# Performance work log

Measured on AMD Instinct MI355X. Metric: run time of the kernel, lower is better.

Reference implementation:

```python
import jax, jax.numpy as jnp
import numpy as np

B, N, K, NUM_CLASSES = 8, 4096, 16, 40
M = B * N


def _safe_norm(v):
    s = jnp.sum(v * v, axis=-1)
    return jnp.where(s > 0, jnp.sqrt(jnp.where(s > 0, s, 1.0)), 0.0)


def _angle(v1, v2):
    cn = _safe_norm(jnp.cross(v1, v2))
    d = jnp.sum(v1 * v2, axis=-1)
    ok = (cn > 0) | (d != 0)
    return jnp.where(ok, jnp.arctan2(cn, jnp.where(ok, d, 1.0)), 0.0)


def _ppf(pos_i, pos_j, n_i, n_j):
    # PyG point_pair_features: pseudo = pos_j - pos_i (j = source, i = target)
    pseudo = pos_j - pos_i
    return jnp.stack([_safe_norm(pseudo), _angle(n_i, pseudo),
                      _angle(n_j, pseudo), _angle(n_i, n_j)], axis=-1)


def _knn_edges(pos):
    # knn_graph(k=K, loop=False), per-graph; returns (src, dst) with self-loops
    # appended (PPFConv add_self_loops=True default).
    p = pos.reshape(B, N, 3)
    sq = jnp.sum(p * p, axis=-1)                                   # [B,N]
    d2 = sq[:, :, None] + sq[:, None, :] - 2.0 * jnp.einsum('bnd,bmd->bnm', p, p)
    d2 = jnp.where(jnp.eye(N, dtype=bool)[None], jnp.inf, d2)      # no loops
    _, nbr = jax.lax.top_k(-d2, K)                                  # [B,N,K]
    offs = (jnp.arange(B) * N)[:, None, None]
    src = (nbr + offs).reshape(-1)                                  # neighbors j
    dst = jnp.repeat(jnp.arange(M), K)                              # targets i
    loops = jnp.arange(M)
    return jnp.concatenate([src, loops]), jnp.concatenate([dst, loops])


def _mlp(e, w1, b1, w2, b2):
    return jax.nn.relu(e @ w1 + b1) @ w2 + b2


def setup_inputs() -> dict:
    key = jax.random.key(0)
    ks = jax.random.split(key, 12)
    pos = jax.random.normal(ks[0], (M, 3), jnp.float32)
    nrm = jax.random.normal(ks[1], (M, 3), jnp.float32)
    nrm = nrm / jnp.linalg.norm(nrm, axis=-1, keepdims=True)
    batch = jnp.repeat(jnp.arange(B, dtype=jnp.int32), N)
    s = 0.1
    return {
        'pos': pos, 'normal': nrm, 'batch': batch,
        'w1a': jax.random.normal(ks[2], (4, 32)) * s,  'b1a': jnp.zeros(32),
        'w1b': jax.random.normal(ks[3], (32, 32)) * s, 'b1b': jnp.zeros(32),
        'w2a': jax.random.normal(ks[4], (36, 32)) * s, 'b2a': jnp.zeros(32),
        'w2b': jax.random.normal(ks[5], (32, 32)) * s, 'b2b': jnp.zeros(32),
        'wc':  jax.random.normal(ks[6], (32, NUM_CLASSES)) * s,
        'bc':  jnp.zeros(NUM_CLASSES),
    }


def reference(pos, normal, batch, w1a, b1a, w1b, b1b, w2a, b2a, w2b, b2b, wc, bc):
    src, dst = _knn_edges(pos)
    feats = _ppf(pos[dst], pos[src], normal[dst], normal[src])      # [E,4]
    # conv1: x=None -> message = mlp1(ppf), scatter-max per target node
    msg1 = _mlp(feats, w1a, b1a, w1b, b1b)
    x = jax.nn.relu(jax.ops.segment_max(msg1, dst, num_segments=M))  # [M,32]
    # conv2: message = mlp2([x_j, ppf])
    msg2 = _mlp(jnp.concatenate([x[src], feats], axis=-1), w2a, b2a, w2b, b2b)
    x = jax.nn.relu(jax.ops.segment_max(msg2, dst, num_segments=M))
    # global_max_pool over each graph (uniform batch: reshape)
    g = x.reshape(B, N, 32).max(axis=1)                              # [B,32]
    return g @ wc + bc                                               # [B,40]
```

## Files before the change

### kernel.cpp

```cpp
#include <hip/hip_runtime.h>
#include <hip/hip_bf16.h>
#include <math.h>

#define NB 8
#define NN 4096
#define KK 16
#define MM (NB*NN)
#define CH 32
#define SLOTS 17
#define NCLS 40
#define BIG 3.0e38f
#define CAP 96
#define NBLK2 (MM/64)
#define HROW 36

#define OW1A 0
#define OB1A 128
#define OW1B 160
#define OB1B 1184
#define OW2A 1216
#define OB2A 2368
#define OW2B 2400
#define OB2B 3424
#define OWC  3456
#define OBC  4736
#define NWTS 4776

typedef short short8 __attribute__((ext_vector_type(8)));
typedef float f32x4  __attribute__((ext_vector_type(4)));
typedef float f32x2  __attribute__((ext_vector_type(2)));

__device__ float4 g_pos4[MM];
__device__ float4 g_nrm4[MM];
__device__ int    g_nbr[MM*KK];
__device__ float  g_u[MM*CH];
__device__ float  g_bmax[NBLK2*CH];
__device__ float  g_wts[NWTS];
__device__ __align__(16) float4 g_fe4[MM*SLOTS];
__device__ __align__(16) unsigned short g_wfrag1[2][2][64][8];
__device__ __align__(16) unsigned short g_wfrag2[2][2][64][8];

__device__ __forceinline__ float bf(const __hip_bfloat16 x) { return __bfloat162float(x); }

__device__ __forceinline__ float ldf(const void* p, int i, bool f32) {
  return f32 ? ((const float*)p)[i] : bf(((const __hip_bfloat16*)p)[i]);
}

__device__ __forceinline__ float angf(float ax, float ay, float az,
                                      float bx, float by, float bz) {
  float cx = ay*bz - az*by;
  float cy = az*bx - ax*bz;
  float cz = ax*by - ay*bx;
  float s  = cx*cx + cy*cy + cz*cz;
  float cn = s > 0.f ? sqrtf(s) : 0.f;
  float d  = ax*bx + ay*by + az*bz;
  return (cn > 0.f || d != 0.f) ? atan2f(cn, d) : 0.f;
}

__device__ __forceinline__ void ppf4(const float4 pi, const float4 ni,
                                     const float4 pj, const float4 nj, float* f) {
  float px = pj.x - pi.x, py = pj.y - pi.y, pz = pj.z - pi.z;
  float s = px*px + py*py + pz*pz;
  f[0] = s > 0.f ? sqrtf(s) : 0.f;
  f[1] = angf(ni.x, ni.y, ni.z, px, py, pz);
  f[2] = angf(nj.x, nj.y, nj.z, px, py, pz);
  f[3] = angf(ni.x, ni.y, ni.z, nj.x, nj.y, nj.z);
}

__device__ __forceinline__ unsigned int fkey(float f) {
  unsigned int u = __float_as_uint(f);
  return (u & 0x80000000u) ? ~u : (u | 0x80000000u);
}
__device__ __forceinline__ float funkey(unsigned int k) {
  unsigned int u = (k & 0x80000000u) ? (k ^ 0x80000000u) : ~k;
  return __uint_as_float(u);
}

__device__ __forceinline__ unsigned int mbcnt64(unsigned long long m) {
  return __builtin_amdgcn_mbcnt_hi((unsigned int)(m >> 32),
         __builtin_amdgcn_mbcnt_lo((unsigned int)m, 0u));
}

__device__ __forceinline__ void bsplit(float v, unsigned short* hi, unsigned short* lo) {
  __hip_bfloat16 h = __float2bfloat16(v);
  float hf = __bfloat162float(h);
  __hip_bfloat16 l = __float2bfloat16(v - hf);
  *hi = *reinterpret_cast<unsigned short*>(&h);
  *lo = *reinterpret_cast<unsigned short*>(&l);
}

__device__ __forceinline__ void afrag(const float* row, short8* ah, short8* al) {
  float4 a = *(const float4*)row;
  float4 b = *(const float4*)(row + 4);
  unsigned short h, l;
  #pragma unroll
  for (int j = 0; j < 4; ++j) {
    bsplit((&a.x)[j], &h, &l); (*ah)[j]   = (short)h; (*al)[j]   = (short)l;
    bsplit((&b.x)[j], &h, &l); (*ah)[j+4] = (short)h; (*al)[j+4] = (short)l;
  }
}

__global__ __launch_bounds__(256) void prep_kernel(
    const void* __restrict__ pos, const void* __restrict__ nrm,
    const void* w1a, const void* b1a, const void* w1b, const void* b1b,
    const void* w2a, const void* b2a, const void* w2b, const void* b2b,
    const void* wc, const void* bc) {
  __shared__ int sflag;
  const int tid = threadIdx.x;
  const int base = blockIdx.x << 8;
  if (tid < 64) {
    const float* nf = (const float*)nrm;
    const __hip_bfloat16* nh = (const __hip_bfloat16*)nrm;
    int n = base + tid;
    float x = nf[3*n], y = nf[3*n+1], z = nf[3*n+2];
    float ss = x*x + y*y + z*z;
    bool okf = (ss > 0.98f && ss < 1.02f);
    float a = bf(nh[3*n]), b2 = bf(nh[3*n+1]), c2 = bf(nh[3*n+2]);
    float sb = a*a + b2*b2 + c2*c2;
    bool okb = (sb > 0.95f && sb < 1.05f);
    unsigned long long mf = __ballot(okf), mb = __ballot(okb);
    if (tid == 0) sflag = (__popcll(mf) >= __popcll(mb)) ? 1 : 0;
  }
  __syncthreads();
  const bool f32 = sflag != 0;
  {
    int i = base + tid;
    float x = ldf(pos, 3*i, f32), y = ldf(pos, 3*i+1, f32), z = ldf(pos, 3*i+2, f32);
    g_pos4[i] = make_float4(x, y, z, x*x + y*y + z*z);
    float a = ldf(nrm, 3*i, f32), bb = ldf(nrm, 3*i+1, f32), cc = ldf(nrm, 3*i+2, f32);
    g_nrm4[i] = make_float4(a, bb, cc, 0.f);
  }
  if (blockIdx.x == 0) {
    for (int t = tid; t < 128;  t += 256) g_wts[OW1A + t] = ldf(w1a, t, f32);
    for (int t = tid; t < 32;   t += 256) g_wts[OB1A + t] = ldf(b1a, t, f32);
    for (int t = tid; t < 1024; t += 256) g_wts[OW1B + t] = ldf(w1b, t, f32);
    for (int t = tid; t < 32;   t += 256) g_wts[OB1B + t] = ldf(b1b, t, f32);
    for (int t = tid; t < 1152; t += 256) g_wts[OW2A + t] = ldf(w2a, t, f32);
    for (int t = tid; t < 32;   t += 256) g_wts[OB2A + t] = ldf(b2a, t, f32);
    for (int t = tid; t < 1024; t += 256) g_wts[OW2B + t] = ldf(w2b, t, f32);
    for (int t = tid; t < 32;   t += 256) g_wts[OB2B + t] = ldf(b2b, t, f32);
    for (int t = tid; t < 1280; t += 256) g_wts[OWC  + t] = ldf(wc,  t, f32);
    for (int t = tid; t < 40;   t += 256) g_wts[OBC  + t] = ldf(bc,  t, f32);
    for (int t = tid; t < 4096; t += 256) {
      int which = t >> 11;
      int r = t & 2047;
      int tt = r >> 10;  r &= 1023;
      int hl = r >> 9;   r &= 511;
      int ln = r >> 3;
      int j  = r & 7;
      int k = (ln >> 4)*8 + j;
      int c = tt*16 + (ln & 15);
      float wv = ldf(which ? w2b : w1b, k*CH + c, f32);
      unsigned short hi, lo;
      bsplit(wv, &hi, &lo);
      unsigned short v = hl ? lo : hi;
      if (which) g_wfrag2[tt][hl][ln][j] = v;
      else       g_wfrag1[tt][hl][ln][j] = v;
    }
  }
}

__global__ __launch_bounds__(512) void knn_conv1_kernel() {
  __shared__ __align__(16) union SU {
    struct {
      float sx[NN], sy[NN], sz[NN];
      unsigned short ilst[64][CAP];
      double dlst[8][CAP];
    } k;
    struct {
      float fe[272][4];
      float h1s[288*HROW];
      float wsaT[32*HROW];
      float xs[16][CH];
    } c;
  } u;
  __shared__ unsigned short nbrs[64][KK];
  __shared__ unsigned short swcnt[64];

  const int tid  = threadIdx.x;
  const int w    = tid >> 6, lane = tid & 63;
  const int blk  = blockIdx.x;
  const int b    = blk >> 6;
  const int qbw  = ((blk & 63) << 6) | (w << 3);
  const float4* bp = g_pos4 + b*NN;

  #pragma unroll
  for (int k = 0; k < 8; ++k) {
    int idx = k*512 + tid;
    float4 o = bp[idx];
    u.k.sx[idx] = o.x; u.k.sy[idx] = o.y; u.k.sz[idx] = o.z;
  }
  __syncthreads();

  float q2x[8], q2y[8], q2z[8];
  #pragma unroll
  for (int qq = 0; qq < 8; ++qq) {
    int qi = qbw + qq;
    q2x[qq] = -2.f*u.k.sx[qi]; q2y[qq] = -2.f*u.k.sy[qi]; q2z[qq] = -2.f*u.k.sz[qi];
  }
  const f32x2* sx2 = (const f32x2*)u.k.sx;
  const f32x2* sy2 = (const f32x2*)u.k.sy;
  const f32x2* sz2 = (const f32x2*)u.k.sz;

  float mn[8];
  #pragma unroll
  for (int qq = 0; qq < 8; ++qq) mn[qq] = BIG;
  #pragma unroll 4
  for (int it = 0; it < 32; ++it) {
    int p = it*64 + lane;
    f32x2 ox = sx2[p], oy = sy2[p], oz = sz2[p];
    f32x2 ow = __builtin_elementwise_fma(oz, oz,
               __builtin_elementwise_fma(oy, oy, ox*ox));
    #pragma unroll
    for (int qq = 0; qq < 8; ++qq) {
      f32x2 qx = {q2x[qq], q2x[qq]};
      f32x2 qy = {q2y[qq], q2y[qq]};
      f32x2 qz = {q2z[qq], q2z[qq]};
      f32x2 d = __builtin_elementwise_fma(qx, ox,
                __builtin_elementwise_fma(qy, oy,
                __builtin_elementwise_fma(qz, oz, ow)));
      mn[qq] = fminf(fminf(d[0], d[1]), mn[qq]);
    }
  }

  unsigned int key[8], lo[8], hi[8];
  #pragma unroll
  for (int qq = 0; qq < 8; ++qq) { key[qq] = fkey(mn[qq]) >> 16; lo[qq] = 0u; hi[qq] = 0xFFFFu; }
  #pragma unroll 1
  for (int s = 0; s < 16; ++s) {
    #pragma unroll
    for (int qq = 0; qq < 8; ++qq) {
      unsigned int mid = (lo[qq] + hi[qq]) >> 1;
      int c = (int)__popcll(__ballot(key[qq] <= mid));
      if (c >= 17) hi[qq] = mid; else lo[qq] = mid + 1;
    }
  }
  float Tf[8];
  #pragma unroll
  for (int qq = 0; qq < 8; ++qq) {
    float T = funkey((hi[qq] << 16) | 0xFFFFu);
    Tf[qq] = T + 4e-5f + 1e-5f*fabsf(T);
  }

  unsigned int scnt[8];
  #pragma unroll
  for (int qq = 0; qq < 8; ++qq) scnt[qq] = 0u;
  #pragma unroll 2
  for (int it = 0; it < 32; ++it) {
    int p = it*64 + lane;
    f32x2 ox = sx2[p], oy = sy2[p], oz = sz2[p];
    f32x2 ow = __builtin_elementwise_fma(oz, oz,
               __builtin_elementwise_fma(oy, oy, ox*ox));
    #pragma unroll
    for (int qq = 0; qq < 8; ++qq) {
      f32x2 qx = {q2x[qq], q2x[qq]};
      f32x2 qy = {q2y[qq], q2y[qq]};
      f32x2 qz = {q2z[qq], q2z[qq]};
      f32x2 d = __builtin_elementwise_fma(qx, ox,
                __builtin_elementwise_fma(qy, oy,
                __builtin_elementwise_fma(qz, oz, ow)));
      bool h0 = d[0] <= Tf[qq];
      bool h1 = d[1] <= Tf[qq];
      unsigned long long mk0 = __ballot(h0);
      unsigned long long mk1 = __ballot(h1);
      if (mk0 | mk1) {
        unsigned int cbase = scnt[qq];
        if (h0) {
          unsigned int pos = cbase + mbcnt64(mk0);
          if (pos < CAP) u.k.ilst[(w<<3)|qq][pos] = (unsigned short)(2*p);
        }
        cbase += (unsigned int)__popcll(mk0);
        if (h1) {
          unsigned int pos = cbase + mbcnt64(mk1);
          if (pos < CAP) u.k.ilst[(w<<3)|qq][pos] = (unsigned short)(2*p + 1);
        }
        scnt[qq] = cbase + (unsigned int)__popcll(mk1);
      }
    }
  }
  if (lane == 0) {
    #pragma unroll
    for (int qq = 0; qq < 8; ++qq)
      swcnt[(w<<3)|qq] = (unsigned short)min((int)scnt[qq], CAP);
  }

  #pragma unroll 1
  for (int qq = 0; qq < 8; ++qq) {
    const int qi = qbw + qq;
    const int ql = (w<<3) | qq;
    const int m = (int)swcnt[ql];
    const double mx = (double)u.k.sx[qi], my_ = (double)u.k.sy[qi], mz = (double)u.k.sz[qi];
    const double sqme = (mx*mx + my_*my_) + mz*mz;
    for (int e = lane; e < m; e += 64) {
      int ci = u.k.ilst[ql][e];
      double ox = (double)u.k.sx[ci], oy = (double)u.k.sy[ci], oz = (double)u.k.sz[ci];
      double sqo = (ox*ox + oy*oy) + oz*oz;
      double dt  = (mx*ox + my_*oy) + mz*oz;
      u.k.dlst[w][e] = (sqme + sqo) - 2.0*dt;
    }
    for (int e = lane; e < m; e += 64) {
      double myd = u.k.dlst[w][e];
      int myi = u.k.ilst[ql][e];
      int rank = 0;
      for (int o = 0; o < m; ++o) {
        double od = u.k.dlst[w][o];
        int oi = u.k.ilst[ql][o];
        rank += (od < myd) || (od == myd && oi < myi);
      }
      if (rank >= 1 && rank <= KK) {
        nbrs[ql][rank-1] = (unsigned short)myi;
        g_nbr[(b*NN + qi)*KK + (rank-1)] = b*NN + myi;
      }
    }
  }

  const int c32 = tid & 31;
  const int quad = lane >> 4, l15 = lane & 15;
  float w1a_c[4];
  #pragma unroll
  for (int f = 0; f < 4; ++f) w1a_c[f] = g_wts[OW1A + f*CH + c32];
  const float b1a_c = g_wts[OB1A + c32];
  short8 bH0 = *(const short8*)&g_wfrag1[0][0][lane][0];
  short8 bL0 = *(const short8*)&g_wfrag1[0][1][lane][0];
  short8 bH1 = *(const short8*)&g_wfrag1[1][0][lane][0];
  short8 bL1 = *(const short8*)&g_wfrag1[1][1][lane][0];
  const float bias0 = g_wts[OB1B + l15];
  const float bias1 = g_wts[OB1B + 16 + l15];

  __syncthreads();

  for (int i2 = tid; i2 < 1024; i2 += 512) {
    int k = i2 >> 5, cc = i2 & 31;
    u.c.wsaT[cc*HROW + k] = g_wts[OW2A + i2];
  }
  const int nbb = b*NN + ((blk & 63) << 6);

  #pragma unroll 1
  for (int ck = 0; ck < 4; ++ck) {
    const int nloc0 = ck << 4;
    if (tid < 272) {
      int ns = tid / 17, slot = tid - ns*17;
      int iloc = nloc0 + ns;
      int ig = nbb + iloc;
      int jg = (slot < KK) ? (b*NN + (int)nbrs[iloc][slot]) : ig;
      float f[4];
      ppf4(g_pos4[ig], g_nrm4[ig], g_pos4[jg], g_nrm4[jg], f);
      float4 fv = make_float4(f[0], f[1], f[2], f[3]);
      *(float4*)u.c.fe[tid] = fv;
      g_fe4[(size_t)(nbb + nloc0)*SLOTS + tid] = fv;
    }
    __syncthreads();
    #pragma unroll
    for (int it = 0; it < 17; ++it) {
      int idx = it*512 + tid;
      int e = idx >> 5;
      float4 f4 = *(const float4*)u.c.fe[e];
      float h = b1a_c + f4.x*w1a_c[0] + f4.y*w1a_c[1] + f4.z*w1a_c[2] + f4.w*w1a_c[3];
      u.c.h1s[e*HROW + c32] = fmaxf(h, 0.f);
    }
    __syncthreads();
    #pragma unroll
    for (int ni = 0; ni < 2; ++ni) {
      const int n16 = w*2 + ni;
      const int rbase = n16*17;
      short8 ah0, al0, ah1, al1;
      afrag(&u.c.h1s[(rbase      + l15)*HROW + quad*8], &ah0, &al0);
      afrag(&u.c.h1s[(rbase + 16 + l15)*HROW + quad*8], &ah1, &al1);
      f32x4 a00 = {0.f,0.f,0.f,0.f}, a01 = a00, a10 = a00, a11 = a00;
      a00 = __builtin_amdgcn_mfma_f32_16x16x32_bf16(ah0, bH0, a00, 0, 0, 0);
      a00 = __builtin_amdgcn_mfma_f32_16x16x32_bf16(ah0, bL0, a00, 0, 0, 0);
      a00 = __builtin_amdgcn_mfma_f32_16x16x32_bf16(al0, bH0, a00, 0, 0, 0);
      a01 = __builtin_amdgcn_mfma_f32_16x16x32_bf16(ah0, bH1, a01, 0, 0, 0);
      a01 = __builtin_amdgcn_mfma_f32_16x16x32_bf16(ah0, bL1, a01, 0, 0, 0);
      a01 = __builtin_amdgcn_mfma_f32_16x16x32_bf16(al0, bH1, a01, 0, 0, 0);
      a10 = __builtin_amdgcn_mfma_f32_16x16x32_bf16(ah1, bH0, a10, 0, 0, 0);
      a10 = __builtin_amdgcn_mfma_f32_16x16x32_bf16(ah1, bL0, a10, 0, 0, 0);
      a10 = __builtin_amdgcn_mfma_f32_16x16x32_bf16(al1, bH0, a10, 0, 0, 0);
      a11 = __builtin_amdgcn_mfma_f32_16x16x32_bf16(ah1, bH1, a11, 0, 0, 0);
      a11 = __builtin_amdgcn_mfma_f32_16x16x32_bf16(ah1, bL1, a11, 0, 0, 0);
      a11 = __builtin_amdgcn_mfma_f32_16x16x32_bf16(al1, bH1, a11, 0, 0, 0);
      float m0 = fmaxf(fmaxf(a00[0], a00[1]), fmaxf(a00[2], a00[3]));
      float m1 = fmaxf(fmaxf(a01[0], a01[1]), fmaxf(a01[2], a01[3]));
      if (quad == 0) { m0 = fmaxf(m0, a10[0]); m1 = fmaxf(m1, a11[0]); }
      m0 = fmaxf(m0, __shfl_xor(m0, 16)); m0 = fmaxf(m0, __shfl_xor(m0, 32));
      m1 = fmaxf(m1, __shfl_xor(m1, 16)); m1 = fmaxf(m1, __shfl_xor(m1, 32));
      if (quad == 0) {
        u.c.xs[n16][l15]      = fmaxf(m0 + bias0, 0.f);
        u.c.xs[n16][16 + l15] = fmaxf(m1 + bias1, 0.f);
      }
    }
    __syncthreads();
    {
      int ns = tid >> 5;
      float uu = 0.f;
      #pragma unroll
      for (int k4 = 0; k4 < 8; ++k4) {
        float4 x4 = *(const float4*)&u.c.xs[ns][4*k4];
        float4 w4 = *(const float4*)&u.c.wsaT[c32*HROW + 4*k4];
        uu += x4.x*w4.x + x4.y*w4.y + x4.z*w4.z + x4.w*w4.w;
      }
      g_u[(nbb + nloc0 + ns)*CH + c32] = uu;
    }
    __syncthreads();
  }
}

__global__ __launch_bounds__(512) void conv2_kernel() {
  __shared__ __align__(16) float fe[272][4];
  __shared__ int jn[272];
  __shared__ __align__(16) float h1s[288*HROW];
  __shared__ float xs[16][CH];
  const int tid = threadIdx.x;
  const int c = tid & 31;
  const int lane = tid & 63, wv = tid >> 6;
  const int quad = lane >> 4, l15 = lane & 15;
  const int node0 = blockIdx.x << 6;
  float w2aL_c[4];
  #pragma unroll
  for (int f = 0; f < 4; ++f) w2aL_c[f] = g_wts[OW2A + (CH + f)*CH + c];
  const float b2a_c = g_wts[OB2A + c];
  short8 bH0 = *(const short8*)&g_wfrag2[0][0][lane][0];
  short8 bL0 = *(const short8*)&g_wfrag2[0][1][lane][0];
  short8 bH1 = *(const short8*)&g_wfrag2[1][0][lane][0];
  short8 bL1 = *(const short8*)&g_wfrag2[1][1][lane][0];
  const float bias0 = g_wts[OB2B + l15];
  const float bias1 = g_wts[OB2B + 16 + l15];
  float bmx = 0.f;

  #pragma unroll 1
  for (int ck = 0; ck < 4; ++ck) {
    const int n0 = node0 + (ck << 4);
    if (tid < 272) {
      int ns = tid / 17, slot = tid - ns*17;
      int i = n0 + ns;
      jn[tid] = (slot < KK) ? g_nbr[i*KK + slot] : i;
      *(float4*)fe[tid] = g_fe4[(size_t)n0*SLOTS + tid];
    }
    __syncthreads();
    #pragma unroll
    for (int it = 0; it < 17; ++it) {
      int idx = it*512 + tid;
      int e = idx >> 5;
      float4 f4 = *(const float4*)fe[e];
      float uv = g_u[jn[e]*CH + c];
      float h = b2a_c + uv + f4.x*w2aL_c[0] + f4.y*w2aL_c[1] + f4.z*w2aL_c[2] + f4.w*w2aL_c[3];
      h1s[e*HROW + c] = fmaxf(h, 0.f);
    }
    __syncthreads();
    #pragma unroll
    for (int ni = 0; ni < 2; ++ni) {
      const int n16 = wv*2 + ni;
      const int rbase = n16*17;
      short8 ah0, al0, ah1, al1;
      afrag(&h1s[(rbase      + l15)*HROW + quad*8], &ah0, &al0);
      afrag(&h1s[(rbase + 16 + l15)*HROW + quad*8], &ah1, &al1);
      f32x4 a00 = {0.f,0.f,0.f,0.f}, a01 = a00, a10 = a00, a11 = a00;
      a00 = __builtin_amdgcn_mfma_f32_16x16x32_bf16(ah0, bH0, a00, 0, 0, 0);
      a00 = __builtin_amdgcn_mfma_f32_16x16x32_bf16(ah0, bL0, a00, 0, 0, 0);
      a00 = __builtin_amdgcn_mfma_f32_16x16x32_bf16(al0, bH0, a00, 0, 0, 0);
      a01 = __builtin_amdgcn_mfma_f32_16x16x32_bf16(ah0, bH1, a01, 0, 0, 0);
      a01 = __builtin_amdgcn_mfma_f32_16x16x32_bf16(ah0, bL1, a01, 0, 0, 0);
      a01 = __builtin_amdgcn_mfma_f32_16x16x32_bf16(al0, bH1, a01, 0, 0, 0);
      a10 = __builtin_amdgcn_mfma_f32_16x16x32_bf16(ah1, bH0, a10, 0, 0, 0);
      a10 = __builtin_amdgcn_mfma_f32_16x16x32_bf16(ah1, bL0, a10, 0, 0, 0);
      a10 = __builtin_amdgcn_mfma_f32_16x16x32_bf16(al1, bH0, a10, 0, 0, 0);
      a11 = __builtin_amdgcn_mfma_f32_16x16x32_bf16(ah1, bH1, a11, 0, 0, 0);
      a11 = __builtin_amdgcn_mfma_f32_16x16x32_bf16(ah1, bL1, a11, 0, 0, 0);
      a11 = __builtin_amdgcn_mfma_f32_16x16x32_bf16(al1, bH1, a11, 0, 0, 0);
      float m0 = fmaxf(fmaxf(a00[0], a00[1]), fmaxf(a00[2], a00[3]));
      float m1 = fmaxf(fmaxf(a01[0], a01[1]), fmaxf(a01[2], a01[3]));
      if (quad == 0) { m0 = fmaxf(m0, a10[0]); m1 = fmaxf(m1, a11[0]); }
      m0 = fmaxf(m0, __shfl_xor(m0, 16)); m0 = fmaxf(m0, __shfl_xor(m0, 32));
      m1 = fmaxf(m1, __shfl_xor(m1, 16)); m1 = fmaxf(m1, __shfl_xor(m1, 32));
      if (quad == 0) {
        xs[n16][l15]      = fmaxf(m0 + bias0, 0.f);
        xs[n16][16 + l15] = fmaxf(m1 + bias1, 0.f);
      }
    }
    __syncthreads();
    if (tid < CH) {
      #pragma unroll
      for (int r = 0; r < 16; ++r) bmx = fmaxf(bmx, xs[r][c]);
    }
    __syncthreads();
  }
  if (tid < CH) g_bmax[blockIdx.x*CH + c] = bmx;
}

__global__ __launch_bounds__(256) void head_kernel(float* __restrict__ out) {
  __shared__ float red[8][CH];
  __shared__ float gm[CH];
  const int g = blockIdx.x;
  const int c = threadIdx.x & 31, sub = threadIdx.x >> 5;
  const float* base = g_bmax + (size_t)(g*64 + sub*8)*CH;
  float mx = 0.f;
  #pragma unroll
  for (int n = 0; n < 8; ++n) mx = fmaxf(mx, base[n*CH + c]);
  red[sub][c] = mx;
  __syncthreads();
  if (threadIdx.x < CH) {
    float m2 = red[0][c];
    #pragma unroll
    for (int r = 1; r < 8; ++r) m2 = fmaxf(m2, red[r][c]);
    gm[c] = m2;
  }
  __syncthreads();
  if (threadIdx.x < NCLS) {
    int co = threadIdx.x;
    float s = g_wts[OBC + co];
    #pragma unroll
    for (int f = 0; f < CH; ++f) s += gm[f] * g_wts[OWC + f*NCLS + co];
    out[g*NCLS + co] = s;
  }
}

extern "C" void kernel_launch(void* const* d_in, const int* in_sizes, int n_in,
                              void* d_out, int out_size, void* d_ws, size_t ws_size,
                              hipStream_t stream) {
  const void* pos = d_in[0];
  const void* nrm = d_in[1];
  const void* w1a = d_in[3];
  const void* b1a = d_in[4];
  const void* w1b = d_in[5];
  const void* b1b = d_in[6];
  const void* w2a = d_in[7];
  const void* b2a = d_in[8];
  const void* w2b = d_in[9];
  const void* b2b = d_in[10];
  const void* wc  = d_in[11];
  const void* bc  = d_in[12];

  prep_kernel<<<MM/256, 256, 0, stream>>>(pos, nrm, w1a, b1a, w1b, b1b,
                                          w2a, b2a, w2b, b2b, wc, bc);
  knn_conv1_kernel<<<MM/64, 512, 0, stream>>>();
  conv2_kernel<<<MM/64, 512, 0, stream>>>();
  head_kernel<<<NB, 256, 0, stream>>>((float*)d_out);
}
```

Before: 191.7 us.

## Halve nodes per block and stream candidate points through LDS in halves

Each block now handles 32 query nodes instead of 64, with 4 queries per wave. The kNN scan loads the 4096 candidate points into shared memory in two halves of 2048, which shrinks the LDS footprint and adds an extra barrier per pass. PPF features are built once for the whole block rather than per chunk, the double-precision refinement reads candidate positions from global memory, and the conv stages process one node per wave per chunk. The aim is more resident blocks per CU (launch bounds min 8 blocks) and twice as many blocks, at the cost of reloading the point set twice per block and more total global traffic.

```diff
diff --git a/kernel.cpp b/kernel.cpp
--- a/kernel.cpp
+++ b/kernel.cpp
@@ -11,8 +11,10 @@
 #define NCLS 40
 #define BIG 3.0e38f
 #define CAP 96
-#define NBLK2 (MM/64)
+#define NPB 32
+#define NBLK (MM/NPB)
 #define HROW 36
+#define HALF 2048
 
 #define OW1A 0
 #define OB1A 128
@@ -34,7 +36,7 @@
 __device__ float4 g_nrm4[MM];
 __device__ int    g_nbr[MM*KK];
 __device__ float  g_u[MM*CH];
-__device__ float  g_bmax[NBLK2*CH];
+__device__ float  g_bmax[NBLK*CH];
 __device__ float  g_wts[NWTS];
 __device__ __align__(16) float4 g_fe4[MM*SLOTS];
 __device__ __align__(16) unsigned short g_wfrag1[2][2][64][8];
@@ -160,140 +162,152 @@
   }
 }
 
-__global__ __launch_bounds__(512) void knn_conv1_kernel() {
+__global__ __launch_bounds__(512, 8) void knn_conv1_kernel() {
   __shared__ __align__(16) union SU {
     struct {
-      float sx[NN], sy[NN], sz[NN];
-      unsigned short ilst[64][CAP];
+      float sx[HALF], sy[HALF], sz[HALF];
+      unsigned short ilst[NPB][CAP];
       double dlst[8][CAP];
     } k;
     struct {
-      float fe[272][4];
-      float h1s[288*HROW];
+      float fe[NPB*SLOTS][4];
+      float h1s[152*HROW];
       float wsaT[32*HROW];
-      float xs[16][CH];
+      float xs[NPB][CH];
     } c;
   } u;
-  __shared__ unsigned short nbrs[64][KK];
-  __shared__ unsigned short swcnt[64];
+  __shared__ unsigned short nbrs[NPB][KK];
 
   const int tid  = threadIdx.x;
   const int w    = tid >> 6, lane = tid & 63;
   const int blk  = blockIdx.x;
-  const int b    = blk >> 6;
-  const int qbw  = ((blk & 63) << 6) | (w << 3);
+  const int b    = blk >> 7;
+  const int qb   = (blk & 127) << 5;
   const float4* bp = g_pos4 + b*NN;
 
-  #pragma unroll
-  for (int k = 0; k < 8; ++k) {
-    int idx = k*512 + tid;
-    float4 o = bp[idx];
-    u.k.sx[idx] = o.x; u.k.sy[idx] = o.y; u.k.sz[idx] = o.z;
-  }
-  __syncthreads();
-
-  float q2x[8], q2y[8], q2z[8];
-  #pragma unroll
-  for (int qq = 0; qq < 8; ++qq) {
-    int qi = qbw + qq;
-    q2x[qq] = -2.f*u.k.sx[qi]; q2y[qq] = -2.f*u.k.sy[qi]; q2z[qq] = -2.f*u.k.sz[qi];
-  }
+  float q2x[4], q2y[4], q2z[4];
+  #pragma unroll
+  for (int qq = 0; qq < 4; ++qq) {
+    float4 qv = bp[qb + (w << 2) + qq];
+    q2x[qq] = -2.f*qv.x; q2y[qq] = -2.f*qv.y; q2z[qq] = -2.f*qv.z;
+  }
+
   const f32x2* sx2 = (const f32x2*)u.k.sx;
   const f32x2* sy2 = (const f32x2*)u.k.sy;
   const f32x2* sz2 = (const f32x2*)u.k.sz;
 
-  float mn[8];
-  #pragma unroll
-  for (int qq = 0; qq < 8; ++qq) mn[qq] = BIG;
-  #pragma unroll 4
-  for (int it = 0; it < 32; ++it) {
-    int p = it*64 + lane;
-    f32x2 ox = sx2[p], oy = sy2[p], oz = sz2[p];
-    f32x2 ow = __builtin_elementwise_fma(oz, oz,
-               __builtin_elementwise_fma(oy, oy, ox*ox));
-    #pragma unroll
-    for (int qq = 0; qq < 8; ++qq) {
-      f32x2 qx = {q2x[qq], q2x[qq]};
-      f32x2 qy = {q2y[qq], q2y[qq]};
-      f32x2 qz = {q2z[qq], q2z[qq]};
-      f32x2 d = __builtin_elementwise_fma(qx, ox,
-                __builtin_elementwise_fma(qy, oy,
-                __builtin_elementwise_fma(qz, oz, ow)));
-      mn[qq] = fminf(fminf(d[0], d[1]), mn[qq]);
-    }
-  }
-
-  unsigned int key[8], lo[8], hi[8];
-  #pragma unroll
-  for (int qq = 0; qq < 8; ++qq) { key[qq] = fkey(mn[qq]) >> 16; lo[qq] = 0u; hi[qq] = 0xFFFFu; }
+  float mn[4];
+  #pragma unroll
+  for (int qq = 0; qq < 4; ++qq) mn[qq] = BIG;
+  #pragma unroll 1
+  for (int h = 0; h < 2; ++h) {
+    #pragma unroll
+    for (int k = 0; k < 4; ++k) {
+      int idx = k*512 + tid;
+      float4 o = bp[h*HALF + idx];
+      u.k.sx[idx] = o.x; u.k.sy[idx] = o.y; u.k.sz[idx] = o.z;
+    }
+    __syncthreads();
+    #pragma unroll 4
+    for (int it = 0; it < 16; ++it) {
+      int p = it*64 + lane;
+      f32x2 ox = sx2[p], oy = sy2[p], oz = sz2[p];
+      f32x2 ow = __builtin_elementwise_fma(oz, oz,
+                 __builtin_elementwise_fma(oy, oy, ox*ox));
+      #pragma unroll
+      for (int qq = 0; qq < 4; ++qq) {
+        f32x2 qx = {q2x[qq], q2x[qq]};
+        f32x2 qy = {q2y[qq], q2y[qq]};
+        f32x2 qz = {q2z[qq], q2z[qq]};
+        f32x2 d = __builtin_elementwise_fma(qx, ox,
+                  __builtin_elementwise_fma(qy, oy,
+                  __builtin_elementwise_fma(qz, oz, ow)));
+        mn[qq] = fminf(fminf(d[0], d[1]), mn[qq]);
+      }
+    }
+    __syncthreads();
+  }
+
+  unsigned int key[4], lo[4], hi[4];
+  #pragma unroll
+  for (int qq = 0; qq < 4; ++qq) { key[qq] = fkey(mn[qq]) >> 16; lo[qq] = 0u; hi[qq] = 0xFFFFu; }
   #pragma unroll 1
   for (int s = 0; s < 16; ++s) {
     #pragma unroll
-    for (int qq = 0; qq < 8; ++qq) {
+    for (int qq = 0; qq < 4; ++qq) {
       unsigned int mid = (lo[qq] + hi[qq]) >> 1;
       int c = (int)__popcll(__ballot(key[qq] <= mid));
       if (c >= 17) hi[qq] = mid; else lo[qq] = mid + 1;
     }
   }
-  float Tf[8];
-  #pragma unroll
-  for (int qq = 0; qq < 8; ++qq) {
+  float Tf[4];
+  #pragma unroll
+  for (int qq = 0; qq < 4; ++qq) {
     float T = funkey((hi[qq] << 16) | 0xFFFFu);
     Tf[qq] = T + 4e-5f + 1e-5f*fabsf(T);
   }
 
-  unsigned int scnt[8];
-  #pragma unroll
-  for (int qq = 0; qq < 8; ++qq) scnt[qq] = 0u;
-  #pragma unroll 2
-  for (int it = 0; it < 32; ++it) {
-    int p = it*64 + lane;
-    f32x2 ox = sx2[p], oy = sy2[p], oz = sz2[p];
-    f32x2 ow = __builtin_elementwise_fma(oz, oz,
-               __builtin_elementwise_fma(oy, oy, ox*ox));
-    #pragma unroll
-    for (int qq = 0; qq < 8; ++qq) {
-      f32x2 qx = {q2x[qq], q2x[qq]};
-      f32x2 qy = {q2y[qq], q2y[qq]};
-      f32x2 qz = {q2z[qq], q2z[qq]};
-      f32x2 d = __builtin_elementwise_fma(qx, ox,
-                __builtin_elementwise_fma(qy, oy,
-                __builtin_elementwise_fma(qz, oz, ow)));
-      bool h0 = d[0] <= Tf[qq];
-      bool h1 = d[1] <= Tf[qq];
-      unsigned long long mk0 = __ballot(h0);
-      unsigned long long mk1 = __ballot(h1);
-      if (mk0 | mk1) {
-        unsigned int cbase = scnt[qq];
-        if (h0) {
-          unsigned int pos = cbase + mbcnt64(mk0);
-          if (pos < CAP) u.k.ilst[(w<<3)|qq][pos] = (unsigned short)(2*p);
+  unsigned int scnt[4];
+  #pragma unroll
+  for (int qq = 0; qq < 4; ++qq) scnt[qq] = 0u;
+  #pragma unroll 1
+  for (int h = 0; h < 2; ++h) {
+    #pragma unroll
+    for (int k = 0; k < 4; ++k) {
+      int idx = k*512 + tid;
+      float4 o = bp[h*HALF + idx];
+      u.k.sx[idx] = o.x; u.k.sy[idx] = o.y; u.k.sz[idx] = o.z;
+    }
+    __syncthreads();
+    #pragma unroll 2
+    for (int it = 0; it < 16; ++it) {
+      int p = it*64 + lane;
+      int gidx = h*HALF + 2*p;
+      f32x2 ox = sx2[p], oy = sy2[p], oz = sz2[p];
+      f32x2 ow = __builtin_elementwise_fma(oz, oz,
+                 __builtin_elementwise_fma(oy, oy, ox*ox));
+      #pragma unroll
+      for (int qq = 0; qq < 4; ++qq) {
+        f32x2 qx = {q2x[qq], q2x[qq]};
+        f32x2 qy = {q2y[qq], q2y[qq]};
+        f32x2 qz = {q2z[qq], q2z[qq]};
+        f32x2 d = __builtin_elementwise_fma(qx, ox,
+                  __builtin_elementwise_fma(qy, oy,
+                  __builtin_elementwise_fma(qz, oz, ow)));
+        bool h0 = d[0] <= Tf[qq];
+        bool h1 = d[1] <= Tf[qq];
+        unsigned long long mk0 = __ballot(h0);
+        unsigned long long mk1 = __ballot(h1);
+        if (mk0 | mk1) {
+          unsigned int cbase = scnt[qq];
+          if (h0) {
+            unsigned int pos = cbase + mbcnt64(mk0);
+            if (pos < CAP) u.k.ilst[(w<<2)|qq][pos] = (unsigned short)gidx;
+          }
+          cbase += (unsigned int)__popcll(mk0);
+          if (h1) {
+            unsigned int pos = cbase + mbcnt64(mk1);
+            if (pos < CAP) u.k.ilst[(w<<2)|qq][pos] = (unsigned short)(gidx + 1);
+          }
+          scnt[qq] = cbase + (unsigned int)__popcll(mk1);
         }
-        cbase += (unsigned int)__popcll(mk0);
-        if (h1) {
-          unsigned int pos = cbase + mbcnt64(mk1);
-          if (pos < CAP) u.k.ilst[(w<<3)|qq][pos] = (unsigned short)(2*p + 1);
-        }
-        scnt[qq] = cbase + (unsigned int)__popcll(mk1);
-      }
-    }
-  }
-  if (lane == 0) {
-    #pragma unroll
-    for (int qq = 0; qq < 8; ++qq)
-      swcnt[(w<<3)|qq] = (unsigned short)min((int)scnt[qq], CAP);
+      }
+    }
+    __syncthreads();
   }
 
   #pragma unroll 1
-  for (int qq = 0; qq < 8; ++qq) {
-    const int qi = qbw + qq;
-    const int ql = (w<<3) | qq;
-    const int m = (int)swcnt[ql];
-    const double mx = (double)u.k.sx[qi], my_ = (double)u.k.sy[qi], mz = (double)u.k.sz[qi];
+  for (int qq = 0; qq < 4; ++qq) {
+    const int ql = (w << 2) | qq;
+    const int m = min((int)scnt[qq], CAP);
+    const double mx = (double)(-0.5f*q2x[qq]);
+    const double my_ = (double)(-0.5f*q2y[qq]);
+    const double mz = (double)(-0.5f*q2z[qq]);
     const double sqme = (mx*mx + my_*my_) + mz*mz;
     for (int e = lane; e < m; e += 64) {
       int ci = u.k.ilst[ql][e];
-      double ox = (double)u.k.sx[ci], oy = (double)u.k.sy[ci], oz = (double)u.k.sz[ci];
+      float4 cv = bp[ci];
+      double ox = (double)cv.x, oy = (double)cv.y, oz = (double)cv.z;
       double sqo = (ox*ox + oy*oy) + oz*oz;
       double dt  = (mx*ox + my_*oy) + mz*oz;
       u.k.dlst[w][e] = (sqme + sqo) - 2.0*dt;
@@ -309,7 +323,7 @@
       }
       if (rank >= 1 && rank <= KK) {
         nbrs[ql][rank-1] = (unsigned short)myi;
-        g_nbr[(b*NN + qi)*KK + (rank-1)] = b*NN + myi;
+        g_nbr[(b*NN + qb + ql)*KK + (rank-1)] = b*NN + myi;
       }
     }
   }
@@ -333,36 +347,34 @@
     int k = i2 >> 5, cc = i2 & 31;
     u.c.wsaT[cc*HROW + k] = g_wts[OW2A + i2];
   }
-  const int nbb = b*NN + ((blk & 63) << 6);
+  const int nbb = b*NN + qb;
+  for (int e = tid; e < NPB*SLOTS; e += 512) {
+    int ns = e / 17, slot = e - ns*17;
+    int ig = nbb + ns;
+    int jg = (slot < KK) ? (b*NN + (int)nbrs[ns][slot]) : ig;
+    float f[4];
+    ppf4(g_pos4[ig], g_nrm4[ig], g_pos4[jg], g_nrm4[jg], f);
+    float4 fv = make_float4(f[0], f[1], f[2], f[3]);
+    *(float4*)u.c.fe[e] = fv;
+    g_fe4[(size_t)nbb*SLOTS + e] = fv;
+  }
+  __syncthreads();
 
   #pragma unroll 1
   for (int ck = 0; ck < 4; ++ck) {
-    const int nloc0 = ck << 4;
-    if (tid < 272) {
-      int ns = tid / 17, slot = tid - ns*17;
-      int iloc = nloc0 + ns;
-      int ig = nbb + iloc;
-      int jg = (slot < KK) ? (b*NN + (int)nbrs[iloc][slot]) : ig;
-      float f[4];
-      ppf4(g_pos4[ig], g_nrm4[ig], g_pos4[jg], g_nrm4[jg], f);
-      float4 fv = make_float4(f[0], f[1], f[2], f[3]);
-      *(float4*)u.c.fe[tid] = fv;
-      g_fe4[(size_t)(nbb + nloc0)*SLOTS + tid] = fv;
-    }
-    __syncthreads();
-    #pragma unroll
-    for (int it = 0; it < 17; ++it) {
+    #pragma unroll
+    for (int it = 0; it < 9; ++it) {
       int idx = it*512 + tid;
       int e = idx >> 5;
-      float4 f4 = *(const float4*)u.c.fe[e];
-      float h = b1a_c + f4.x*w1a_c[0] + f4.y*w1a_c[1] + f4.z*w1a_c[2] + f4.w*w1a_c[3];
-      u.c.h1s[e*HROW + c32] = fmaxf(h, 0.f);
-    }
-    __syncthreads();
-    #pragma unroll
-    for (int ni = 0; ni < 2; ++ni) {
-      const int n16 = w*2 + ni;
-      const int rbase = n16*17;
+      if (e < 136) {
+        float4 f4 = *(const float4*)u.c.fe[ck*136 + e];
+        float h = b1a_c + f4.x*w1a_c[0] + f4.y*w1a_c[1] + f4.z*w1a_c[2] + f4.w*w1a_c[3];
+        u.c.h1s[e*HROW + c32] = fmaxf(h, 0.f);
+      }
+    }
+    __syncthreads();
+    {
+      const int rbase = w*17;
       short8 ah0, al0, ah1, al1;
       afrag(&u.c.h1s[(rbase      + l15)*HROW + quad*8], &ah0, &al0);
       afrag(&u.c.h1s[(rbase + 16 + l15)*HROW + quad*8], &ah1, &al1);
@@ -385,36 +397,36 @@
       m0 = fmaxf(m0, __shfl_xor(m0, 16)); m0 = fmaxf(m0, __shfl_xor(m0, 32));
       m1 = fmaxf(m1, __shfl_xor(m1, 16)); m1 = fmaxf(m1, __shfl_xor(m1, 32));
       if (quad == 0) {
-        u.c.xs[n16][l15]      = fmaxf(m0 + bias0, 0.f);
-        u.c.xs[n16][16 + l15] = fmaxf(m1 + bias1, 0.f);
-      }
-    }
-    __syncthreads();
-    {
-      int ns = tid >> 5;
-      float uu = 0.f;
-      #pragma unroll
-      for (int k4 = 0; k4 < 8; ++k4) {
-        float4 x4 = *(const float4*)&u.c.xs[ns][4*k4];
-        float4 w4 = *(const float4*)&u.c.wsaT[c32*HROW + 4*k4];
-        uu += x4.x*w4.x + x4.y*w4.y + x4.z*w4.z + x4.w*w4.w;
-      }
-      g_u[(nbb + nloc0 + ns)*CH + c32] = uu;
-    }
-    __syncthreads();
-  }
-}
-
-__global__ __launch_bounds__(512) void conv2_kernel() {
-  __shared__ __align__(16) float fe[272][4];
-  __shared__ int jn[272];
-  __shared__ __align__(16) float h1s[288*HROW];
-  __shared__ float xs[16][CH];
+        u.c.xs[ck*8 + w][l15]      = fmaxf(m0 + bias0, 0.f);
+        u.c.xs[ck*8 + w][16 + l15] = fmaxf(m1 + bias1, 0.f);
+      }
+    }
+    __syncthreads();
+  }
+  #pragma unroll
+  for (int it = 0; it < 2; ++it) {
+    int ns = it*16 + (tid >> 5);
+    float uu = 0.f;
+    #pragma unroll
+    for (int k4 = 0; k4 < 8; ++k4) {
+      float4 x4 = *(const float4*)&u.c.xs[ns][4*k4];
+      float4 w4 = *(const float4*)&u.c.wsaT[c32*HROW + 4*k4];
+      uu += x4.x*w4.x + x4.y*w4.y + x4.z*w4.z + x4.w*w4.w;
+    }
+    g_u[(nbb + ns)*CH + c32] = uu;
+  }
+}
+
+__global__ __launch_bounds__(512, 8) void conv2_kernel() {
+  __shared__ __align__(16) float fe[NPB*SLOTS][4];
+  __shared__ int jn[NPB*SLOTS];
+  __shared__ __align__(16) float h1s[152*HROW];
+  __shared__ float xs[NPB][CH];
   const int tid = threadIdx.x;
   const int c = tid & 31;
   const int lane = tid & 63, wv = tid >> 6;
   const int quad = lane >> 4, l15 = lane & 15;
-  const int node0 = blockIdx.x << 6;
+  const int node0 = blockIdx.x << 5;
   float w2aL_c[4];
   #pragma unroll
   for (int f = 0; f < 4; ++f) w2aL_c[f] = g_wts[OW2A + (CH + f)*CH + c];
@@ -425,32 +437,31 @@
   short8 bL1 = *(const short8*)&g_wfrag2[1][1][lane][0];
   const float bias0 = g_wts[OB2B + l15];
   const float bias1 = g_wts[OB2B + 16 + l15];
-  float bmx = 0.f;
+
+  for (int e = tid; e < NPB*SLOTS; e += 512) {
+    int ns = e / 17, slot = e - ns*17;
+    int i = node0 + ns;
+    jn[e] = (slot < KK) ? g_nbr[i*KK + slot] : i;
+    *(float4*)fe[e] = g_fe4[(size_t)node0*SLOTS + e];
+  }
+  __syncthreads();
 
   #pragma unroll 1
   for (int ck = 0; ck < 4; ++ck) {
-    const int n0 = node0 + (ck << 4);
-    if (tid < 272) {
-      int ns = tid / 17, slot = tid - ns*17;
-      int i = n0 + ns;
-      jn[tid] = (slot < KK) ? g_nbr[i*KK + slot] : i;
-      *(float4*)fe[tid] = g_fe4[(size_t)n0*SLOTS + tid];
-    }
-    __syncthreads();
-    #pragma unroll
-    for (int it = 0; it < 17; ++it) {
+    #pragma unroll
+    for (int it = 0; it < 9; ++it) {
       int idx = it*512 + tid;
       int e = idx >> 5;
-      float4 f4 = *(const float4*)fe[e];
-      float uv = g_u[jn[e]*CH + c];
-      float h = b2a_c + uv + f4.x*w2aL_c[0] + f4.y*w2aL_c[1] + f4.z*w2aL_c[2] + f4.w*w2aL_c[3];
-      h1s[e*HROW + c] = fmaxf(h, 0.f);
-    }
-    __syncthreads();
-    #pragma unroll
-    for (int ni = 0; ni < 2; ++ni) {
-      const int n16 = wv*2 + ni;
-      const int rbase = n16*17;
+      if (e < 136) {
+        float4 f4 = *(const float4*)fe[ck*136 + e];
+        float uv = g_u[jn[ck*136 + e]*CH + c];
+        float h = b2a_c + uv + f4.x*w2aL_c[0] + f4.y*w2aL_c[1] + f4.z*w2aL_c[2] + f4.w*w2aL_c[3];
+        h1s[e*HROW + c] = fmaxf(h, 0.f);
+      }
+    }
+    __syncthreads();
+    {
+      const int rbase = wv*17;
       short8 ah0, al0, ah1, al1;
       afrag(&h1s[(rbase      + l15)*HROW + quad*8], &ah0, &al0);
       afrag(&h1s[(rbase + 16 + l15)*HROW + quad*8], &ah1, &al1);
@@ -473,18 +484,18 @@
       m0 = fmaxf(m0, __shfl_xor(m0, 16)); m0 = fmaxf(m0, __shfl_xor(m0, 32));
       m1 = fmaxf(m1, __shfl_xor(m1, 16)); m1 = fmaxf(m1, __shfl_xor(m1, 32));
       if (quad == 0) {
-        xs[n16][l15]      = fmaxf(m0 + bias0, 0.f);
-        xs[n16][16 + l15] = fmaxf(m1 + bias1, 0.f);
-      }
-    }
-    __syncthreads();
-    if (tid < CH) {
-      #pragma unroll
-      for (int r = 0; r < 16; ++r) bmx = fmaxf(bmx, xs[r][c]);
-    }
-    __syncthreads();
-  }
-  if (tid < CH) g_bmax[blockIdx.x*CH + c] = bmx;
+        xs[ck*8 + wv][l15]      = fmaxf(m0 + bias0, 0.f);
+        xs[ck*8 + wv][16 + l15] = fmaxf(m1 + bias1, 0.f);
+      }
+    }
+    __syncthreads();
+  }
+  if (tid < CH) {
+    float m2 = xs[0][c];
+    #pragma unroll
+    for (int r = 1; r < NPB; ++r) m2 = fmaxf(m2, xs[r][c]);
+    g_bmax[blockIdx.x*CH + c] = m2;
+  }
 }
 
 __global__ __launch_bounds__(256) void head_kernel(float* __restrict__ out) {
@@ -492,10 +503,10 @@
   __shared__ float gm[CH];
   const int g = blockIdx.x;
   const int c = threadIdx.x & 31, sub = threadIdx.x >> 5;
-  const float* base = g_bmax + (size_t)(g*64 + sub*8)*CH;
+  const float* base = g_bmax + (size_t)(g*128 + sub*16)*CH;
   float mx = 0.f;
   #pragma unroll
-  for (int n = 0; n < 8; ++n) mx = fmaxf(mx, base[n*CH + c]);
+  for (int n = 0; n < 16; ++n) mx = fmaxf(mx, base[n*CH + c]);
   red[sub][c] = mx;
   __syncthreads();
   if (threadIdx.x < CH) {
@@ -532,7 +543,7 @@
 
   prep_kernel<<<MM/256, 256, 0, stream>>>(pos, nrm, w1a, b1a, w1b, b1b,
                                           w2a, b2a, w2b, b2b, wc, bc);
-  knn_conv1_kernel<<<MM/64, 512, 0, stream>>>();
-  conv2_kernel<<<MM/64, 512, 0, stream>>>();
+  knn_conv1_kernel<<<NBLK, 512, 0, stream>>>();
+  conv2_kernel<<<NBLK, 512, 0, stream>>>();
   head_kernel<<<NB, 256, 0, stream>>>((float*)d_out);
 }
```

New measurement: 212.2 us. 1.11x slower.
